# Kernel optimization log

Measured on AMD Instinct MI355X. Metric: run time of the kernel, lower is better.

Reference implementation:

```python
import jax, jax.numpy as jnp
import numpy as np

B, L, H, N, CH = 8, 2048, 512, 64, 1


def setup_inputs() -> dict:
    key = jax.random.key(0)
    ks = jax.random.split(key, 7)
    # S4D-Lin style init: w = -0.5 + i*pi*n, with slight noise on the real part
    w_re = -(0.5 + 0.1 * jax.random.uniform(ks[0], (H, N), dtype=jnp.float32))
    w_im = jnp.broadcast_to(jnp.pi * jnp.arange(N, dtype=jnp.float32), (H, N)).copy()
    C_re = jax.random.normal(ks[1], (CH, H, N), dtype=jnp.float32)
    C_im = jax.random.normal(ks[2], (CH, H, N), dtype=jnp.float32)
    D = jax.random.normal(ks[3], (CH, H), dtype=jnp.float32)
    # log-uniform dt in [1e-3, 1e-1]
    log_dt = jax.random.uniform(ks[4], (H,), dtype=jnp.float32,
                                minval=jnp.log(1e-3), maxval=jnp.log(1e-1))
    dt = jnp.exp(log_dt)
    u = jax.random.normal(ks[5], (B, L, H), dtype=jnp.float32)
    return {"u": u, "w_re": w_re, "w_im": w_im, "C_re": C_re,
            "C_im": C_im, "D": D, "dt": dt}


def reference(u, w_re, w_im, C_re, C_im, D, dt):
    # u: [B, L, H] -> [B, H, L]
    uT = jnp.swapaxes(u, -1, -2)
    l = uT.shape[-1]
    h = dt.shape[-1]
    w = (w_re + 1j * w_im).astype(jnp.complex64)          # [t, n]
    v = h // w.shape[0]
    w = jnp.tile(w, (v, 1))                                # [h, n]
    C = (C_re + 1j * C_im).astype(jnp.complex64)           # [c, h, n]
    # --- kernel generation ---
    dtA = w * dt[:, None]                                  # [h, n]
    K = jnp.arange(l) * dtA[..., None]                     # [h, n, l]
    Cs = C * ((jnp.exp(dtA) - 1.0) / w)                    # [c, h, n]
    k = 2.0 * jnp.einsum('chn,hnl->chl', Cs, jnp.exp(K)).real  # [c, h, l]
    # --- FFT convolution ---
    k_f = jnp.fft.rfft(k, n=2 * l - 1)                     # [c, h, l]
    u_f = jnp.fft.rfft(uT, n=2 * l - 1)                    # [B, h, l]
    y_f = jnp.einsum('...hl,chl->...chl', u_f, k_f)        # [B, c, h, l]
    y = jnp.fft.irfft(y_f, n=2 * l)[..., :l]               # [B, c, h, l]
    # skip connection
    y = y + jnp.einsum('...hl,ch->...chl', uT, D)
    # '... c h l -> ... l c h'
    return jnp.moveaxis(y, (-3, -2, -1), (-2, -1, -3))
```

## Files before the change

kernel.cpp:

```cpp
#include <hip/hip_runtime.h>
#include <hip/hip_bf16.h>
#include <math.h>


namespace {
constexpr int cB = 8;
constexpr int cL = 2048;
constexpr int cH = 512;
constexpr int cN = 64;
constexpr int M1 = 4095;
constexpr int M2 = 4096;
constexpr int BH = cB * cH;
constexpr int MA = BH + cH;

constexpr size_t S0   = 2 * ((size_t)cH * cN * 6);
constexpr size_t S_B1 = S0;
constexpr size_t S_A  = S_B1 + (size_t)4096 * 2048;
constexpr size_t S_T2 = S_A  + (size_t)MA * 2048;
constexpr size_t S_U  = S_T2 + (size_t)2048 * 4096;
}

typedef __attribute__((ext_vector_type(8))) short short8;
typedef __attribute__((ext_vector_type(4))) float f32x4;

static __device__ inline short f2bf(float x) {
    __hip_bfloat16 h = __float2bfloat16(x);
    return *reinterpret_cast<short*>(&h);
}
static __device__ inline float bf2f(short s) {
    return __uint_as_float(((unsigned int)(unsigned short)s) << 16);
}
static __device__ __forceinline__ void load_lds16(const short* g, short* l) {
    __builtin_amdgcn_global_load_lds(
        (const __attribute__((address_space(1))) void*)g,
        (__attribute__((address_space(3))) void*)l, 16, 0, 0);
}
#define WAIT_LGKM0() do { asm volatile("s_waitcnt lgkmcnt(0)" ::: "memory"); \
                          __builtin_amdgcn_sched_barrier(0); } while (0)
#define WAIT_VM(n)   do { asm volatile("s_waitcnt vmcnt(" #n ")" ::: "memory"); \
                          __builtin_amdgcn_sched_barrier(0); } while (0)
#define BAR() __builtin_amdgcn_s_barrier()

__global__ __launch_bounds__(256) void k_tabs(short* __restrict__ Wb)
{
    int tid = threadIdx.x;
    if (blockIdx.x < 2048) {
        int j  = blockIdx.x;
        int base = (j < 1024) ? 4 * j : (j == 1024 ? 2 : 4 * (2048 - j) + 2);
        int t0 = tid * 8;
        int p0 = (int)(((long)j * t0) % M1);
        float c, s, cs, ss;
        sincosf((6.283185307179586f / (float)M1) * (float)p0, &s, &c);
        sincosf((6.283185307179586f / (float)M1) * (float)j,  &ss, &cs);
        short8 vc, vs;
#pragma unroll
        for (int i = 0; i < 8; ++i) {
            vc[i] = f2bf(c); vs[i] = f2bf(s);
            float tr = c * cs - s * ss;
            s = c * ss + s * cs;
            c = tr;
        }
        *(short8*)&Wb[S_B1 + (size_t)base       * 2048 + t0] = vc;
        *(short8*)&Wb[S_B1 + (size_t)(base + 1) * 2048 + t0] = vs;
    } else {
        int r   = blockIdx.x - 2048;
        int p   = r >> 10, tau = r & 1023;
        int t   = 2 * tau + p;
        int k0  = tid * 8;
        float stepang = (6.283185307179586f / (float)M2) * (float)t;
        float cs, ss; sincosf(stepang, &ss, &cs);
        short8 v;
        if (k0 < 1024) {
            int ph = (k0 * t) & (M2 - 1);
            float c, s; sincosf((6.283185307179586f / (float)M2) * (float)ph, &s, &c);
#pragma unroll
            for (int i = 0; i < 8; ++i) {
                v[i] = f2bf(c);
                float tr = c * cs - s * ss;
                s = c * ss + s * cs;
                c = tr;
            }
        } else {
            int j0 = k0 - 1024;
            int ph = (j0 * t) & (M2 - 1);
            float c, s; sincosf((6.283185307179586f / (float)M2) * (float)ph, &s, &c);
#pragma unroll
            for (int i = 0; i < 8; ++i) {
                int k = k0 + i;
                v[i] = (k == 1024) ? f2bf((tau & 1) ? -1.f : 1.f) : f2bf(s);
                float tr = c * cs - s * ss;
                s = c * ss + s * cs;
                c = tr;
            }
        }
        *(short8*)&Wb[S_T2 + (size_t)r * 2048 + k0] = v;
    }
}

__global__ __launch_bounds__(256) void k_trans(const float* __restrict__ u,
                                               short* __restrict__ Wb)
{
    __shared__ float tile[64][65];
    int t0 = blockIdx.x * 64;
    int h0 = blockIdx.y * 64;
    int b  = blockIdx.z;
    int cx = threadIdx.x & 63, r0 = threadIdx.x >> 6;
#pragma unroll
    for (int i = 0; i < 16; ++i) {
        int row = r0 + i * 4;
        tile[row][cx] = u[((size_t)b * cL + t0 + row) * cH + h0 + cx];
    }
    __syncthreads();
    short* A = Wb + S_A;
#pragma unroll
    for (int i = 0; i < 16; ++i) {
        int hrow = r0 + i * 4;
        A[(size_t)(b * cH + h0 + hrow) * 2048 + t0 + cx] = f2bf(tile[cx][hrow]);
    }
}

__global__ __launch_bounds__(256) void k_kgen(
    const float* __restrict__ w_re, const float* __restrict__ w_im,
    const float* __restrict__ C_re, const float* __restrict__ C_im,
    const float* __restrict__ dt, short* __restrict__ Wb)
{
    __shared__ float md[cN * 6];
    int h = blockIdx.x, tid = threadIdx.x;
    if (tid < cN) {
        int idx = h * cN + tid;
        double dtv = dt[h];
        double wr = w_re[idx], wi = w_im[idx];
        double ar = wr * dtv, ai = wi * dtv;
        double er = exp(ar);
        double zs, zc; sincos(ai, &zs, &zc);
        double zr = er * zc, zi = er * zs;
        double nr = zr - 1.0, ni = zi;
        double inv = 1.0 / (wr * wr + wi * wi);
        double gr = (nr * wr + ni * wi) * inv;
        double gi = (ni * wr - nr * wi) * inv;
        double cr = C_re[idx], ci = C_im[idx];
        md[tid*6+0] = (float)(cr * gr - ci * gi);
        md[tid*6+1] = (float)(cr * gi + ci * gr);
        md[tid*6+2] = (float)zr; md[tid*6+3] = (float)zi;
        md[tid*6+4] = (float)ar; md[tid*6+5] = (float)ai;
    }
    __syncthreads();
    int t0 = tid * 8;
    float acc[8] = {0.f, 0.f, 0.f, 0.f, 0.f, 0.f, 0.f, 0.f};
    for (int n = 0; n < cN; ++n) {
        float csr = md[n*6+0], csi = md[n*6+1];
        float zr  = md[n*6+2], zi  = md[n*6+3];
        float ar  = md[n*6+4], ai  = md[n*6+5];
        float mag = expf(ar * (float)t0);
        double ph = fmod((double)ai * (double)t0, 6.283185307179586);
        float s, c; sincosf((float)ph, &s, &c);
        float pr = mag * c, pi = mag * s;
#pragma unroll
        for (int i = 0; i < 8; ++i) {
            acc[i] += csr * pr - csi * pi;
            float tr = pr * zr - pi * zi;
            pi = pr * zi + pi * zr;
            pr = tr;
        }
    }
    short8 v;
#pragma unroll
    for (int i = 0; i < 8; ++i) v[i] = f2bf(2.f * acc[i]);
    *reinterpret_cast<short8*>(&Wb[S_A + (size_t)(BH + h) * 2048 + t0]) = v;
}

#define MFMA16(AR, BR, ACC) \
    _Pragma("unroll") for (int kk = 0; kk < 2; ++kk) \
    _Pragma("unroll") for (int ni = 0; ni < 2; ++ni) \
    _Pragma("unroll") for (int mi = 0; mi < 4; ++mi) \
        ACC[mi][ni] = __builtin_amdgcn_mfma_f32_16x16x32_bf16(AR[mi][kk], BR[ni][kk], ACC[mi][ni], 0, 0, 0);

__device__ __forceinline__ void gemm2p_core(
    const short* __restrict__ Ag, int lda,
    const short* __restrict__ Bg, int ldb,
    int m0, int n0, int nt, short* lds, f32x4 (&acc)[4][4][2])
{
    const int tid  = threadIdx.x;
    const int wave = tid >> 6, lane = tid & 63;
    const int wm = wave >> 2, wn = wave & 3;
    const int lm = lane & 15, lk = lane >> 4;
    const int srow8 = lane >> 3;
    const int scol  = (lane & 7) * 8;

    auto stage = [&](const short* G, int ldg, int row0, int half, int kt, int sb) {
        short* l0 = lds + sb + (size_t)((kt & 1) * 2 + half) * 8192;
#pragma unroll
        for (int q = 0; q < 2; ++q) {
            int chunk = wave * 2 + q;
            int r = chunk * 8 + srow8;
            int c = scol ^ ((r & 7) << 3);
            load_lds16(G + (size_t)(row0 + half * 128 + r) * ldg + kt * 64 + c,
                       l0 + chunk * 512);
        }
    };
    auto rdA = [&](int qa, int kt, int mi, int kk) -> short8 {
        int rl = wm * 64 + mi * 16 + lm;
        int c  = (kk * 32 + lk * 8) ^ ((rl & 7) << 3);
        return *(const short8*)(lds + (size_t)((kt & 1) * 2 + qa) * 8192 + rl * 64 + c);
    };
    auto rdB = [&](int qb, int kt, int ni, int kk) -> short8 {
        int rl = wn * 32 + ni * 16 + lm;
        int c  = (kk * 32 + lk * 8) ^ ((rl & 7) << 3);
        return *(const short8*)(lds + 32768 + (size_t)((kt & 1) * 2 + qb) * 8192 + rl * 64 + c);
    };

    stage(Ag, lda, m0, 0, 0, 0);
    stage(Bg, ldb, n0, 0, 0, 32768);
    stage(Bg, ldb, n0, 1, 0, 32768);
    stage(Ag, lda, m0, 1, 0, 0);
    stage(Ag, lda, m0, 0, 1, 0);
    stage(Bg, ldb, n0, 0, 1, 32768);
    stage(Bg, ldb, n0, 1, 1, 32768);
    stage(Ag, lda, m0, 1, 1, 0);
    WAIT_VM(8);
    BAR();

    short8 a0[4][2], a1[4][2], b0[2][2], b1[2][2];
#pragma unroll
    for (int mi = 0; mi < 4; ++mi) { a0[mi][0] = rdA(0, 0, mi, 0); a0[mi][1] = rdA(0, 0, mi, 1); }
#pragma unroll
    for (int ni = 0; ni < 2; ++ni) { b0[ni][0] = rdB(0, 0, ni, 0); b0[ni][1] = rdB(0, 0, ni, 1); }

    for (int t = 0; t < nt; ++t) {
        const bool st = (t + 2 < nt);
        const bool rd = (t + 1 < nt);
#pragma unroll
        for (int ni = 0; ni < 2; ++ni) { b1[ni][0] = rdB(1, t, ni, 0); b1[ni][1] = rdB(1, t, ni, 1); }
#pragma unroll
        for (int mi = 0; mi < 4; ++mi) { a1[mi][0] = rdA(1, t, mi, 0); a1[mi][1] = rdA(1, t, mi, 1); }
        BAR();
        WAIT_LGKM0();
        __builtin_amdgcn_s_setprio(1);
        MFMA16(a0, b0, acc[0]);
        MFMA16(a0, b1, acc[1]);
        __builtin_amdgcn_s_setprio(0);
        BAR();
        if (st) {
            stage(Ag, lda, m0, 0, t + 2, 0);
            stage(Bg, ldb, n0, 0, t + 2, 32768);
            stage(Bg, ldb, n0, 1, t + 2, 32768);
            stage(Ag, lda, m0, 1, t + 2, 0);
            WAIT_VM(8);
        } else {
            WAIT_VM(0);
        }
        BAR();
        __builtin_amdgcn_s_setprio(1);
        MFMA16(a1, b1, acc[3]);
        MFMA16(a1, b0, acc[2]);
        __builtin_amdgcn_s_setprio(0);
        if (rd) {
#pragma unroll
            for (int mi = 0; mi < 4; ++mi) { a0[mi][0] = rdA(0, t + 1, mi, 0); a0[mi][1] = rdA(0, t + 1, mi, 1); }
#pragma unroll
            for (int ni = 0; ni < 2; ++ni) { b0[ni][0] = rdB(0, t + 1, ni, 0); b0[ni][1] = rdB(0, t + 1, ni, 1); }
        }
    }
}

__global__ __launch_bounds__(512, 2) void k_fwd8(short* __restrict__ Wb)
{
    __shared__ short lds_s[65536];
    int xcd = blockIdx.x & 7, idx = blockIdx.x >> 3;
    const int m0 = (((xcd >> 1) << 2) + (idx >> 3)) * 256;
    const int n0 = (((xcd & 1) << 3) + (idx & 7)) * 256;
    const int tid = threadIdx.x;
    const int wave = tid >> 6, lane = tid & 63;
    const int wm = wave >> 2, wn = wave & 3;
    const int lm = lane & 15, lk = lane >> 4;

    f32x4 acc[4][4][2] = {};
    gemm2p_core(Wb + S_A, 2048, Wb + S_B1, 2048, m0, n0, 32, lds_s, acc);

    short* Uw = Wb + S_U;
    const short* KF = Wb + S_U;
    short (*M)[136] = (short(*)[136])lds_s;
    for (int q = 0; q < 4; ++q) {
        __syncthreads();
#pragma unroll
        for (int mi = 0; mi < 4; ++mi)
#pragma unroll
        for (int ni = 0; ni < 2; ++ni)
#pragma unroll
        for (int r = 0; r < 4; ++r)
            M[wm * 64 + mi * 16 + lk * 4 + r][wn * 32 + ni * 16 + lm] =
                f2bf(acc[q][mi][ni][r]);
        __syncthreads();
        const int pq0 = (n0 >> 2) + (q & 1) * 32;
        int rl = tid >> 2;
        int cp = (tid & 3) * 8;
        int rowg = m0 + (q >> 1) * 128 + rl;
        int h = rowg & (cH - 1);
        int colg = n0 + (q & 1) * 128 + cp * 4;
        short8 kf4[4], m4[4];
#pragma unroll
        for (int w = 0; w < 4; ++w) {
            kf4[w] = *(const short8*)&KF[(size_t)(4096 + h) * 4096 + colg + w * 8];
            m4[w]  = *(const short8*)&M[rl][cp * 4 + w * 8];
        }
        short8 vce, vse, vco, vso;
#pragma unroll
        for (int i = 0; i < 8; ++i) {
            int w = i >> 1, o = (i & 1) * 4;
            float C  = bf2f(m4[w][o]),   S  = bf2f(m4[w][o+1]);
            float C2 = bf2f(m4[w][o+2]), S2 = bf2f(m4[w][o+3]);
            float Ck  = bf2f(kf4[w][o]),   Sk  = bf2f(kf4[w][o+1]);
            float Ck2 = bf2f(kf4[w][o+2]), Sk2 = bf2f(kf4[w][o+3]);
            int pp = pq0 + cp + i;
            float scp = (pp == 0 ? 1.0f : 2.0f) * (1.0f / (float)M2);
            float scq = 2.0f / (float)M2;
            float yrp = scp * (Ck * C - Sk * S);
            float yip = scp * (Ck * S + Sk * C);
            float yrq = scq * (Ck2 * C2 - Sk2 * S2);
            float yiq = scq * (Ck2 * S2 + Sk2 * C2);
            float ce, co, se, so;
            if (pp == 0) { ce = yrp; co = yrp; se = yrq; so = yiq; }
            else { ce = yrp + yrq; co = yrp - yrq; se = yip - yiq; so = yip + yiq; }
            vce[i] = f2bf(ce); vco[i] = f2bf(co);
            vse[i] = f2bf(se); vso[i] = f2bf(so);
        }
        size_t base = (size_t)rowg * 4096;
        int kx = pq0 + cp;
        *(short8*)&Uw[base + kx]        = vce;
        *(short8*)&Uw[base + 1024 + kx] = vse;
        *(short8*)&Uw[base + 2048 + kx] = vco;
        *(short8*)&Uw[base + 3072 + kx] = vso;
    }
}

__global__ __launch_bounds__(256, 2) void k_kfg(short* __restrict__ Wb)
{
    __shared__ __align__(16) short As[64][32];
    __shared__ __align__(16) short Bs[128][32];
    const short* A = Wb + S_A;
    const short* B = Wb + S_B1;
    short* U = Wb + S_U;
    const int tid = threadIdx.x;
    const int m0 = 4096 + blockIdx.y * 64, n0 = blockIdx.x * 128;
    const int wave = tid >> 6, lane = tid & 63;
    const int wr = wave >> 1, wc = wave & 1;
    const int lm = lane & 15, lk = lane >> 4;
    const int srowA = tid >> 2,  scolA = (tid & 3) * 8;
    const int srowB = lane >> 2, scolB = (lane & 3) * 8;

    f32x4 acc[2][4] = {};
    for (int k0 = 0; k0 < 2048; k0 += 32) {
        __syncthreads();
        load_lds16(&A[(size_t)(m0 + srowA) * 2048 + k0 + scolA],
                   &As[0][0] + wave * 512);
#pragma unroll
        for (int q = 0; q < 2; ++q) {
            int chunk = wave * 2 + q;
            load_lds16(&B[(size_t)(n0 + chunk * 16 + srowB) * 2048 + k0 + scolB],
                       &Bs[chunk * 16][0]);
        }
        __syncthreads();
        short8 a[2];
#pragma unroll
        for (int mi = 0; mi < 2; ++mi)
            a[mi] = *(const short8*)&As[wr*32 + mi*16 + lm][lk*8];
#pragma unroll
        for (int ni = 0; ni < 4; ++ni) {
            short8 b = *(const short8*)&Bs[wc*64 + ni*16 + lm][lk*8];
#pragma unroll
            for (int mi = 0; mi < 2; ++mi)
                acc[mi][ni] = __builtin_amdgcn_mfma_f32_16x16x32_bf16(a[mi], b, acc[mi][ni], 0, 0, 0);
        }
    }
#pragma unroll
    for (int mi = 0; mi < 2; ++mi)
#pragma unroll
    for (int ni = 0; ni < 4; ++ni)
#pragma unroll
    for (int r = 0; r < 4; ++r) {
        int row = m0 + wr*32 + mi*16 + lk*4 + r;
        int col = n0 + wc*64 + ni*16 + lm;
        U[(size_t)row * 4096 + col] = f2bf(acc[mi][ni][r]);
    }
}

__global__ __launch_bounds__(512, 1) void k_invB(const float* __restrict__ u,
                                                 const float* __restrict__ Dp,
                                                 short* __restrict__ Wb,
                                                 float* __restrict__ out)
{
    __shared__ short lds_s[57344];
    int xcd = blockIdx.x & 7, idx = blockIdx.x >> 3;
    const int m0 = ((((xcd >> 1) << 2) + (idx >> 3))) * 256;
    const int nj = ((xcd & 1) << 3) + (idx & 7);
    const int p  = nj >> 3;
    const int n0 = (nj & 7) * 128;
    const int tid = threadIdx.x;
    const int wave = tid >> 6, lane = tid & 63;
    const int wm = wave >> 2, wn = wave & 3;
    const int lm = lane & 15, lk = lane >> 4;
    const int srow8 = lane >> 3;
    const int scol  = (lane & 7) * 8;
    constexpr int nt = 32;
    short* lds = lds_s;
    const short* Ag = Wb + S_U + (size_t)p * 2048;
    const short* Bg = Wb + S_T2 + (size_t)p * 1024 * 2048;

    auto stageA = [&](int half, int kt) {
        short* l0 = lds + (size_t)((kt & 1) * 2 + half) * 8192;
#pragma unroll
        for (int q = 0; q < 2; ++q) {
            int chunk = wave * 2 + q;
            int r = chunk * 8 + srow8;
            int c = scol ^ ((r & 7) << 3);
            load_lds16(Ag + (size_t)(m0 + half * 128 + r) * 4096 + kt * 64 + c,
                       l0 + chunk * 512);
        }
    };
    auto stageB = [&](int kt, int slot) {
        short* l0 = lds + 32768 + (size_t)slot * 8192;
#pragma unroll
        for (int q = 0; q < 2; ++q) {
            int chunk = wave * 2 + q;
            int r = chunk * 8 + srow8;
            int c = scol ^ ((r & 7) << 3);
            load_lds16(Bg + (size_t)(n0 + r) * 2048 + kt * 64 + c,
                       l0 + chunk * 512);
        }
    };
    auto rdA = [&](int half, int kt, int mi, int kk) -> short8 {
        int rl = wm * 64 + mi * 16 + lm;
        int c  = (kk * 32 + lk * 8) ^ ((rl & 7) << 3);
        return *(const short8*)(lds + (size_t)((kt & 1) * 2 + half) * 8192 + rl * 64 + c);
    };
    auto rdB = [&](int slot, int ni, int kk) -> short8 {
        int rl = wn * 32 + ni * 16 + lm;
        int c  = (kk * 32 + lk * 8) ^ ((rl & 7) << 3);
        return *(const short8*)(lds + 32768 + (size_t)slot * 8192 + rl * 64 + c);
    };

    f32x4 acc[2][4][2] = {};

    stageA(0, 0);
    stageB(0, 0);
    stageA(1, 0);
    stageA(0, 1);
    stageA(1, 1);
    stageB(1, 1);
    stageB(2, 2);
    WAIT_VM(8);
    BAR();
    short8 a0[4][2], a1[4][2], b[2][2];
#pragma unroll
    for (int mi = 0; mi < 4; ++mi) { a0[mi][0] = rdA(0, 0, mi, 0); a0[mi][1] = rdA(0, 0, mi, 1); }
#pragma unroll
    for (int ni = 0; ni < 2; ++ni) { b[ni][0] = rdB(0, ni, 0); b[ni][1] = rdB(0, ni, 1); }

    int bs = 0;
    for (int t = 0; t < nt; ++t) {
        const bool r1 = (t + 1 < nt);
        const bool s2 = (t + 2 < nt);
        const bool s3 = (t + 3 < nt);
        const bool tail = (t >= nt - 3);
        const int bs2 = (bs == 2) ? 0 : bs + 1;
#pragma unroll
        for (int mi = 0; mi < 4; ++mi) { a1[mi][0] = rdA(1, t, mi, 0); a1[mi][1] = rdA(1, t, mi, 1); }
        BAR();
        WAIT_LGKM0();
        __builtin_amdgcn_s_setprio(1);
        MFMA16(a0, b, acc[0]);
        __builtin_amdgcn_s_setprio(0);
        BAR();
        if (s2) { stageA(1, t + 2); stageA(0, t + 2); }
        if (s3) stageB(t + 3, bs);
        if (tail) { WAIT_VM(0); } else { WAIT_VM(6); }
        BAR();
        __builtin_amdgcn_s_setprio(1);
        MFMA16(a1, b, acc[1]);
        __builtin_amdgcn_s_setprio(0);
        if (r1) {
#pragma unroll
            for (int mi = 0; mi < 4; ++mi) { a0[mi][0] = rdA(0, t + 1, mi, 0); a0[mi][1] = rdA(0, t + 1, mi, 1); }
#pragma unroll
            for (int ni = 0; ni < 2; ++ni) { b[ni][0] = rdB(bs2, ni, 0); b[ni][1] = rdB(bs2, ni, 1); }
        }
        bs = bs2;
    }

    const int b_  = m0 >> 9;
    const int h00 = m0 & 511;
    float (*T)[132] = (float(*)[132])lds_s;
#pragma unroll
    for (int q = 0; q < 2; ++q) {
        __syncthreads();
#pragma unroll
        for (int mi = 0; mi < 4; ++mi)
#pragma unroll
        for (int ni = 0; ni < 2; ++ni) {
            int tl = wn * 32 + ni * 16 + lm;
            int hl = wm * 64 + mi * 16 + lk * 4;
            *(float4*)&T[tl][hl] = *(float4*)&acc[q][mi][ni];
        }
        __syncthreads();
        int hg = h00 + q * 128 + (tid & 31) * 4;
        float4 dv = *(const float4*)&Dp[hg];
#pragma unroll
        for (int it = 0; it < 8; ++it) {
            int tl = (tid >> 5) + it * 16;
            int tg = 2 * (n0 + tl) + p;
            size_t gidx = ((size_t)b_ * cL + tg) * cH + hg;
            float4 uv = *(const float4*)&u[gidx];
            float4 yv = *(float4*)&T[tl][(tid & 31) * 4];
            yv.x += dv.x * uv.x;
            yv.y += dv.y * uv.y;
            yv.z += dv.z * uv.z;
            yv.w += dv.w * uv.w;
            *(float4*)&out[gidx] = yv;
        }
    }
}

extern "C" void kernel_launch(void* const* d_in, const int* in_sizes, int n_in,
                              void* d_out, int out_size, void* d_ws, size_t ws_size,
                              hipStream_t stream) {
    const float* u    = (const float*)d_in[0];
    const float* w_re = (const float*)d_in[1];
    const float* w_im = (const float*)d_in[2];
    const float* C_re = (const float*)d_in[3];
    const float* C_im = (const float*)d_in[4];
    const float* Dp   = (const float*)d_in[5];
    const float* dt   = (const float*)d_in[6];
    float* out = (float*)d_out;
    short* Wb  = (short*)d_ws;

    hipLaunchKernelGGL(k_tabs,  dim3(4096), dim3(256), 0, stream, Wb);
    hipLaunchKernelGGL(k_trans, dim3(cL / 64, cH / 64, cB), dim3(256), 0, stream, u, Wb);
    hipLaunchKernelGGL(k_kgen,  dim3(cH), dim3(256), 0, stream,
                       w_re, w_im, C_re, C_im, dt, Wb);
    hipLaunchKernelGGL(k_kfg,   dim3(32, 8), dim3(256), 0, stream, Wb);
    hipLaunchKernelGGL(k_fwd8,  dim3(256), dim3(512), 0, stream, Wb);
    hipLaunchKernelGGL(k_invB,  dim3(256), dim3(512), 0, stream, u, Dp, Wb, out);
}
```

Before: 190.3 us.

## Switch GEMM cores from 16x16x32 to 32x32x16 bf16 MFMA tiles

Replaces the 16x16x32 MFMA inner loops in the forward GEMM and the inverse GEMM with 32x32x16 MFMAs, remapping LDS fragment reads and the warp-to-output-tile assignment. In the forward kernel each wave now owns a contiguous 128x64 quadrant, so the epilogue writes to the LDS staging buffer only from the owning waves in each quarter pass. The larger MFMA shape is meant to cut LDS read traffic and instruction-issue count per FLOP. In exchange the epilogue serializes the writes onto a subset of waves and uses more accumulator registers per instruction, which may raise register pressure.

After: 204.3 us. 7.3% more time.

```diff
diff --git a/kernel.cpp b/kernel.cpp
--- a/kernel.cpp
+++ b/kernel.cpp
@@ -20,8 +20,9 @@
 constexpr size_t S_U  = S_T2 + (size_t)2048 * 4096;
 }
 
-typedef __attribute__((ext_vector_type(8))) short short8;
-typedef __attribute__((ext_vector_type(4))) float f32x4;
+typedef __attribute__((ext_vector_type(8)))  short short8;
+typedef __attribute__((ext_vector_type(4)))  float f32x4;
+typedef __attribute__((ext_vector_type(16))) float f32x16;
 
 static __device__ inline short f2bf(float x) {
     __hip_bfloat16 h = __float2bfloat16(x);
@@ -175,15 +176,21 @@
     _Pragma("unroll") for (int mi = 0; mi < 4; ++mi) \
         ACC[mi][ni] = __builtin_amdgcn_mfma_f32_16x16x32_bf16(AR[mi][kk], BR[ni][kk], ACC[mi][ni], 0, 0, 0);
 
-__device__ __forceinline__ void gemm2p_core(
+#define MFMA32SET(SA, SB, ACC) \
+    _Pragma("unroll") for (int kk = 0; kk < 2; ++kk) \
+    _Pragma("unroll") for (int ni = 0; ni < 2; ++ni) \
+    _Pragma("unroll") for (int mi = 0; mi < 4; ++mi) \
+        ACC[mi][ni] = __builtin_amdgcn_mfma_f32_32x32x16_bf16(SA[mi][kk], SB[ni][kk], ACC[mi][ni], 0, 0, 0);
+
+__device__ __forceinline__ void gemm2p32(
     const short* __restrict__ Ag, int lda,
     const short* __restrict__ Bg, int ldb,
-    int m0, int n0, int nt, short* lds, f32x4 (&acc)[4][4][2])
+    int m0, int n0, int nt, short* lds, f32x16 (&acc)[4][2])
 {
     const int tid  = threadIdx.x;
     const int wave = tid >> 6, lane = tid & 63;
     const int wm = wave >> 2, wn = wave & 3;
-    const int lm = lane & 15, lk = lane >> 4;
+    const int lr = lane & 31, lh = lane >> 5;
     const int srow8 = lane >> 3;
     const int scol  = (lane & 7) * 8;
 
@@ -198,15 +205,16 @@
                        l0 + chunk * 512);
         }
     };
-    auto rdA = [&](int qa, int kt, int mi, int kk) -> short8 {
-        int rl = wm * 64 + mi * 16 + lm;
-        int c  = (kk * 32 + lk * 8) ^ ((rl & 7) << 3);
-        return *(const short8*)(lds + (size_t)((kt & 1) * 2 + qa) * 8192 + rl * 64 + c);
-    };
-    auto rdB = [&](int qb, int kt, int ni, int kk) -> short8 {
-        int rl = wn * 32 + ni * 16 + lm;
-        int c  = (kk * 32 + lk * 8) ^ ((rl & 7) << 3);
-        return *(const short8*)(lds + 32768 + (size_t)((kt & 1) * 2 + qb) * 8192 + rl * 64 + c);
+    auto rdA = [&](int kt, int mi, int ks) -> short8 {
+        int rl = mi * 32 + lr;
+        int c  = (ks * 16 + lh * 8) ^ ((rl & 7) << 3);
+        return *(const short8*)(lds + (size_t)((kt & 1) * 2 + wm) * 8192 + rl * 64 + c);
+    };
+    auto rdB = [&](int kt, int ni, int ks) -> short8 {
+        int cn = 2 * wn + ni;
+        int rl = (cn & 3) * 32 + lr;
+        int c  = (ks * 16 + lh * 8) ^ ((rl & 7) << 3);
+        return *(const short8*)(lds + 32768 + (size_t)((kt & 1) * 2 + (cn >> 2)) * 8192 + rl * 64 + c);
     };
 
     stage(Ag, lda, m0, 0, 0, 0);
@@ -220,24 +228,23 @@
     WAIT_VM(8);
     BAR();
 
-    short8 a0[4][2], a1[4][2], b0[2][2], b1[2][2];
-#pragma unroll
-    for (int mi = 0; mi < 4; ++mi) { a0[mi][0] = rdA(0, 0, mi, 0); a0[mi][1] = rdA(0, 0, mi, 1); }
-#pragma unroll
-    for (int ni = 0; ni < 2; ++ni) { b0[ni][0] = rdB(0, 0, ni, 0); b0[ni][1] = rdB(0, 0, ni, 1); }
+    short8 s0a[4][2], s0b[2][2], s1a[4][2], s1b[2][2];
+#pragma unroll
+    for (int mi = 0; mi < 4; ++mi) { s0a[mi][0] = rdA(0, mi, 0); s0a[mi][1] = rdA(0, mi, 1); }
+#pragma unroll
+    for (int ni = 0; ni < 2; ++ni) { s0b[ni][0] = rdB(0, ni, 0); s0b[ni][1] = rdB(0, ni, 1); }
 
     for (int t = 0; t < nt; ++t) {
         const bool st = (t + 2 < nt);
         const bool rd = (t + 1 < nt);
 #pragma unroll
-        for (int ni = 0; ni < 2; ++ni) { b1[ni][0] = rdB(1, t, ni, 0); b1[ni][1] = rdB(1, t, ni, 1); }
-#pragma unroll
-        for (int mi = 0; mi < 4; ++mi) { a1[mi][0] = rdA(1, t, mi, 0); a1[mi][1] = rdA(1, t, mi, 1); }
+        for (int mi = 0; mi < 4; ++mi) { s1a[mi][0] = rdA(t, mi, 2); s1a[mi][1] = rdA(t, mi, 3); }
+#pragma unroll
+        for (int ni = 0; ni < 2; ++ni) { s1b[ni][0] = rdB(t, ni, 2); s1b[ni][1] = rdB(t, ni, 3); }
         BAR();
         WAIT_LGKM0();
         __builtin_amdgcn_s_setprio(1);
-        MFMA16(a0, b0, acc[0]);
-        MFMA16(a0, b1, acc[1]);
+        MFMA32SET(s0a, s0b, acc);
         __builtin_amdgcn_s_setprio(0);
         BAR();
         if (st) {
@@ -251,14 +258,13 @@
         }
         BAR();
         __builtin_amdgcn_s_setprio(1);
-        MFMA16(a1, b1, acc[3]);
-        MFMA16(a1, b0, acc[2]);
+        MFMA32SET(s1a, s1b, acc);
         __builtin_amdgcn_s_setprio(0);
         if (rd) {
 #pragma unroll
-            for (int mi = 0; mi < 4; ++mi) { a0[mi][0] = rdA(0, t + 1, mi, 0); a0[mi][1] = rdA(0, t + 1, mi, 1); }
-#pragma unroll
-            for (int ni = 0; ni < 2; ++ni) { b0[ni][0] = rdB(0, t + 1, ni, 0); b0[ni][1] = rdB(0, t + 1, ni, 1); }
+            for (int mi = 0; mi < 4; ++mi) { s0a[mi][0] = rdA(t + 1, mi, 0); s0a[mi][1] = rdA(t + 1, mi, 1); }
+#pragma unroll
+            for (int ni = 0; ni < 2; ++ni) { s0b[ni][0] = rdB(t + 1, ni, 0); s0b[ni][1] = rdB(t + 1, ni, 1); }
         }
     }
 }
@@ -272,24 +278,28 @@
     const int tid = threadIdx.x;
     const int wave = tid >> 6, lane = tid & 63;
     const int wm = wave >> 2, wn = wave & 3;
-    const int lm = lane & 15, lk = lane >> 4;
-
-    f32x4 acc[4][4][2] = {};
-    gemm2p_core(Wb + S_A, 2048, Wb + S_B1, 2048, m0, n0, 32, lds_s, acc);
+    const int lr = lane & 31, lh = lane >> 5;
+
+    f32x16 acc[4][2] = {};
+    gemm2p32(Wb + S_A, 2048, Wb + S_B1, 2048, m0, n0, 32, lds_s, acc);
 
     short* Uw = Wb + S_U;
     const short* KF = Wb + S_U;
     short (*M)[136] = (short(*)[136])lds_s;
     for (int q = 0; q < 4; ++q) {
         __syncthreads();
-#pragma unroll
-        for (int mi = 0; mi < 4; ++mi)
-#pragma unroll
-        for (int ni = 0; ni < 2; ++ni)
-#pragma unroll
-        for (int r = 0; r < 4; ++r)
-            M[wm * 64 + mi * 16 + lk * 4 + r][wn * 32 + ni * 16 + lm] =
-                f2bf(acc[q][mi][ni][r]);
+        if (wm == (q >> 1) && (wn >> 1) == (q & 1)) {
+#pragma unroll
+            for (int mi = 0; mi < 4; ++mi)
+#pragma unroll
+            for (int ni = 0; ni < 2; ++ni)
+#pragma unroll
+            for (int r = 0; r < 16; ++r) {
+                int rowq = mi * 32 + (r & 3) + 8 * (r >> 2) + 4 * lh;
+                int colq = (wn & 1) * 64 + ni * 32 + lr;
+                M[rowq][colq] = f2bf(acc[mi][ni][r]);
+            }
+        }
         __syncthreads();
         const int pq0 = (n0 >> 2) + (q & 1) * 32;
         int rl = tid >> 2;
@@ -398,7 +408,7 @@
     const int tid = threadIdx.x;
     const int wave = tid >> 6, lane = tid & 63;
     const int wm = wave >> 2, wn = wave & 3;
-    const int lm = lane & 15, lk = lane >> 4;
+    const int lr = lane & 31, lh = lane >> 5;
     const int srow8 = lane >> 3;
     const int scol  = (lane & 7) * 8;
     constexpr int nt = 32;
@@ -428,18 +438,18 @@
                        l0 + chunk * 512);
         }
     };
-    auto rdA = [&](int half, int kt, int mi, int kk) -> short8 {
-        int rl = wm * 64 + mi * 16 + lm;
-        int c  = (kk * 32 + lk * 8) ^ ((rl & 7) << 3);
+    auto rdA32 = [&](int half, int kt, int mi, int ks) -> short8 {
+        int rl = wm * 64 + mi * 32 + lr;
+        int c  = (ks * 16 + lh * 8) ^ ((rl & 7) << 3);
         return *(const short8*)(lds + (size_t)((kt & 1) * 2 + half) * 8192 + rl * 64 + c);
     };
-    auto rdB = [&](int slot, int ni, int kk) -> short8 {
-        int rl = wn * 32 + ni * 16 + lm;
-        int c  = (kk * 32 + lk * 8) ^ ((rl & 7) << 3);
+    auto rdB32 = [&](int slot, int ks) -> short8 {
+        int rl = wn * 32 + lr;
+        int c  = (ks * 16 + lh * 8) ^ ((rl & 7) << 3);
         return *(const short8*)(lds + 32768 + (size_t)slot * 8192 + rl * 64 + c);
     };
 
-    f32x4 acc[2][4][2] = {};
+    f32x16 acc[2][2] = {};
 
     stageA(0, 0);
     stageB(0, 0);
@@ -450,11 +460,13 @@
     stageB(2, 2);
     WAIT_VM(8);
     BAR();
-    short8 a0[4][2], a1[4][2], b[2][2];
-#pragma unroll
-    for (int mi = 0; mi < 4; ++mi) { a0[mi][0] = rdA(0, 0, mi, 0); a0[mi][1] = rdA(0, 0, mi, 1); }
-#pragma unroll
-    for (int ni = 0; ni < 2; ++ni) { b[ni][0] = rdB(0, ni, 0); b[ni][1] = rdB(0, ni, 1); }
+    short8 a0[2][4], a1[2][4], b[4];
+#pragma unroll
+    for (int mi = 0; mi < 2; ++mi)
+#pragma unroll
+        for (int ks = 0; ks < 4; ++ks) a0[mi][ks] = rdA32(0, 0, mi, ks);
+#pragma unroll
+    for (int ks = 0; ks < 4; ++ks) b[ks] = rdB32(0, ks);
 
     int bs = 0;
     for (int t = 0; t < nt; ++t) {
@@ -464,11 +476,17 @@
         const bool tail = (t >= nt - 3);
         const int bs2 = (bs == 2) ? 0 : bs + 1;
 #pragma unroll
-        for (int mi = 0; mi < 4; ++mi) { a1[mi][0] = rdA(1, t, mi, 0); a1[mi][1] = rdA(1, t, mi, 1); }
+        for (int mi = 0; mi < 2; ++mi)
+#pragma unroll
+            for (int ks = 0; ks < 4; ++ks) a1[mi][ks] = rdA32(1, t, mi, ks);
         BAR();
         WAIT_LGKM0();
         __builtin_amdgcn_s_setprio(1);
-        MFMA16(a0, b, acc[0]);
+#pragma unroll
+        for (int ks = 0; ks < 4; ++ks)
+#pragma unroll
+        for (int mi = 0; mi < 2; ++mi)
+            acc[0][mi] = __builtin_amdgcn_mfma_f32_32x32x16_bf16(a0[mi][ks], b[ks], acc[0][mi], 0, 0, 0);
         __builtin_amdgcn_s_setprio(0);
         BAR();
         if (s2) { stageA(1, t + 2); stageA(0, t + 2); }
@@ -476,13 +494,19 @@
         if (tail) { WAIT_VM(0); } else { WAIT_VM(6); }
         BAR();
         __builtin_amdgcn_s_setprio(1);
-        MFMA16(a1, b, acc[1]);
+#pragma unroll
+        for (int ks = 0; ks < 4; ++ks)
+#pragma unroll
+        for (int mi = 0; mi < 2; ++mi)
+            acc[1][mi] = __builtin_amdgcn_mfma_f32_32x32x16_bf16(a1[mi][ks], b[ks], acc[1][mi], 0, 0, 0);
         __builtin_amdgcn_s_setprio(0);
         if (r1) {
 #pragma unroll
-            for (int mi = 0; mi < 4; ++mi) { a0[mi][0] = rdA(0, t + 1, mi, 0); a0[mi][1] = rdA(0, t + 1, mi, 1); }
-#pragma unroll
-            for (int ni = 0; ni < 2; ++ni) { b[ni][0] = rdB(bs2, ni, 0); b[ni][1] = rdB(bs2, ni, 1); }
+            for (int mi = 0; mi < 2; ++mi)
+#pragma unroll
+                for (int ks = 0; ks < 4; ++ks) a0[mi][ks] = rdA32(0, t + 1, mi, ks);
+#pragma unroll
+            for (int ks = 0; ks < 4; ++ks) b[ks] = rdB32(bs2, ks);
         }
         bs = bs2;
     }
@@ -494,12 +518,14 @@
     for (int q = 0; q < 2; ++q) {
         __syncthreads();
 #pragma unroll
-        for (int mi = 0; mi < 4; ++mi)
-#pragma unroll
-        for (int ni = 0; ni < 2; ++ni) {
-            int tl = wn * 32 + ni * 16 + lm;
-            int hl = wm * 64 + mi * 16 + lk * 4;
-            *(float4*)&T[tl][hl] = *(float4*)&acc[q][mi][ni];
+        for (int mi = 0; mi < 2; ++mi)
+#pragma unroll
+        for (int g = 0; g < 4; ++g) {
+            int tl = wn * 32 + lr;
+            int hl = wm * 64 + mi * 32 + g * 8 + lh * 4;
+            float4 v4 = make_float4(acc[q][mi][g*4], acc[q][mi][g*4+1],
+                                    acc[q][mi][g*4+2], acc[q][mi][g*4+3]);
+            *(float4*)&T[tl][hl] = v4;
         }
         __syncthreads();
         int hg = h00 + q * 128 + (tid & 31) * 4;
```
